# Kernel tuning notes

Hardware: AMD Instinct MI355X
Metric: run time of the kernel (lower is better)

Reference implementation:

```python
import jax, jax.numpy as jnp
import numpy as np

N_NODES = 100000
N_EDGES = 3200000
IN_DIM, HD_DIM, OUT_DIM = 128, 64, 32


def setup_inputs() -> dict:
    key = jax.random.key(0)
    ks = jax.random.split(key, 8)
    x = jax.random.normal(ks[0], (N_NODES, IN_DIM), dtype=jnp.float32)
    drop_u = jax.random.uniform(ks[1], (N_NODES, IN_DIM), dtype=jnp.float32)
    adj_val = jax.random.uniform(ks[2], (N_EDGES,), dtype=jnp.float32)
    adj_row = jax.random.randint(ks[3], (N_EDGES,), 0, N_NODES, dtype=jnp.int32)
    adj_col = jax.random.randint(ks[4], (N_EDGES,), 0, N_NODES, dtype=jnp.int32)
    W0 = jax.random.normal(ks[5], (IN_DIM, HD_DIM), dtype=jnp.float32) * (1.0 / np.sqrt(IN_DIM))
    b0 = jnp.zeros((HD_DIM,), dtype=jnp.float32)
    W1 = jax.random.normal(ks[6], (HD_DIM, OUT_DIM), dtype=jnp.float32) * (1.0 / np.sqrt(HD_DIM))
    b1 = jnp.zeros((OUT_DIM,), dtype=jnp.float32)
    return {"x": x, "drop_u": drop_u, "adj_val": adj_val, "adj_row": adj_row,
            "adj_col": adj_col, "W0": W0, "b0": b0, "W1": W1, "b1": b1}


def _spmm(val, row, col, h):
    # sparse [N,N] @ dense [N,D]: out[i] = sum_{e: row[e]=i} val[e] * h[col[e]]
    gathered = val[:, None] * h[col]          # [E, D] irregular gather
    return jax.ops.segment_sum(gathered, row, num_segments=N_NODES)


def reference(x, drop_u, adj_val, adj_row, adj_col, W0, b0, W1, b1):
    # dropout p=0.5 (training): keep where u >= 0.5, scale by 1/(1-p)=2
    mask = (drop_u >= 0.5).astype(x.dtype) * 2.0
    h = x * mask
    h = h @ W0 + b0                     # li0: [N, hd]
    h = _spmm(adj_val, adj_row, adj_col, h)
    h = jax.nn.relu(h)
    h = h @ W1 + b1                     # li1: [N, out]
    out = _spmm(adj_val, adj_row, adj_col, h)
    return out
```

## Files before the change

kernel.cpp:

```cpp
#include <hip/hip_runtime.h>

#define NN 100000
#define NE 3200000
#define EB 4096
#define NBP 782
#define BSH 9
#define BRW 512
#define NBK 196
#define CAP 17408

typedef short short8 __attribute__((ext_vector_type(8)));
typedef float f32x4 __attribute__((ext_vector_type(4)));

static __device__ __forceinline__ unsigned short f2bf(float f) {
  union { float f; unsigned int u; } c; c.f = f;
  unsigned int r = c.u + 0x7FFFu + ((c.u >> 16) & 1u);
  return (unsigned short)(r >> 16);
}
static __device__ __forceinline__ float lo16(unsigned int w) {
  union { unsigned int u; float f; } c; c.u = w << 16; return c.f;
}
static __device__ __forceinline__ float hi16(unsigned int w) {
  union { unsigned int u; float f; } c; c.u = w & 0xFFFF0000u; return c.f;
}


__global__ __launch_bounds__(256) void k_binit(int* __restrict__ bcur) {
  int t = threadIdx.x;
  if (t < NBK) bcur[t] = t * CAP;
}

__global__ __launch_bounds__(512) void k_part(const int* __restrict__ row,
                                              const int* __restrict__ col,
                                              const float* __restrict__ val,
                                              int* __restrict__ bcur,
                                              uint2* __restrict__ tmp) {
  __shared__ uint2 stage[EB];
  __shared__ int dst[EB];
  __shared__ int h[NBK];
  __shared__ int bex[NBK];
  __shared__ int win[NBK];
  __shared__ int c2[NBK];
  __shared__ int sc[512];
  int t = threadIdx.x;
  int e0 = blockIdx.x * EB;
  int n = min(EB, NE - e0);
  if (t < NBK) { h[t] = 0; c2[t] = 0; }
  __syncthreads();
  for (int i = t; i < n; i += 512) atomicAdd(&h[row[e0 + i] >> BSH], 1);
  __syncthreads();
  int v = (t < NBK) ? h[t] : 0;
  sc[t] = v;
  __syncthreads();
  for (int off = 1; off < 512; off <<= 1) {
    int a = (t >= off) ? sc[t - off] : 0;
    __syncthreads();
    sc[t] += a;
    __syncthreads();
  }
  int ex = sc[t] - v;
  if (t < NBK) {
    bex[t] = ex;
    win[t] = v ? atomicAdd(&bcur[t], v) : 0;
  }
  __syncthreads();
  for (int i = t; i < n; i += 512) {
    int e = e0 + i;
    int r = row[e];
    unsigned int c = (unsigned int)col[e];
    float vv = val[e];
    int b = r >> BSH;
    int rank = atomicAdd(&c2[b], 1);
    int s_ = bex[b] + rank;
    uint2 w;
    w.x = __float_as_uint(vv);
    w.y = ((unsigned int)(r & (BRW - 1)) << 17) | c;
    stage[s_] = w;
    dst[s_] = win[b] + rank;
  }
  __syncthreads();
  for (int i = t; i < n; i += 512) tmp[dst[i]] = stage[i];
}

__global__ __launch_bounds__(1024) void k_bsort(const int* __restrict__ bcur,
                                                const uint2* __restrict__ tmp,
                                                uint2* __restrict__ vc,
                                                int* __restrict__ rps,
                                                int* __restrict__ rpe) {
  __shared__ int cnt[BRW];
  __shared__ int pre[BRW];
  __shared__ int c2[BRW];
  int t = threadIdx.x;
  int b = blockIdx.x;
  int s0 = b * CAP;
  int n = bcur[b] - s0;
  if (t < BRW) { cnt[t] = 0; c2[t] = 0; }
  __syncthreads();
  const unsigned int* tmpy = (const unsigned int*)tmp;
  for (int i = t; i < n; i += 1024)
    atomicAdd(&cnt[tmpy[2 * (s0 + i) + 1] >> 17], 1);
  __syncthreads();
  int v = (t < BRW) ? cnt[t] : 0;
  if (t < BRW) pre[t] = v;
  __syncthreads();
  for (int off = 1; off < BRW; off <<= 1) {
    int a = (t >= off && t < BRW) ? pre[t - off] : 0;
    __syncthreads();
    if (t < BRW) pre[t] += a;
    __syncthreads();
  }
  if (t < BRW) {
    int ex = pre[t] - v;
    int r = (b << BSH) + t;
    if (r < NN) { rps[r] = s0 + ex; rpe[r] = s0 + ex + v; }
    pre[t] = ex;
  }
  __syncthreads();
  for (int i = t; i < n; i += 1024) {
    uint2 w = tmp[s0 + i];
    int rl = (int)(w.y >> 17);
    int rank = atomicAdd(&c2[rl], 1);
    int pos = s0 + pre[rl] + rank;
    uint2 o;
    o.x = w.x;
    o.y = w.y & 0x1FFFFu;
    vc[pos] = o;
  }
}

__global__ __launch_bounds__(256) void k_wcvt(const float* __restrict__ W0,
                                              unsigned short* __restrict__ W0bT,
                                              const float* __restrict__ W1,
                                              unsigned short* __restrict__ W1bT) {
  int idx = blockIdx.x * 256 + threadIdx.x;
  if (idx < 8192) {
    int n = idx >> 7, k = idx & 127;
    W0bT[idx] = f2bf(W0[(size_t)k * 64 + n]);
  } else if (idx < 8192 + 2048) {
    int i2 = idx - 8192;
    int n = i2 >> 6, k = i2 & 63;
    W1bT[i2] = f2bf(W1[(size_t)k * 32 + n]);
  }
}


__global__ __launch_bounds__(256) void k_gemm0(const float* __restrict__ x,
                                               const float* __restrict__ u,
                                               const unsigned short* __restrict__ W0bT,
                                               const float* __restrict__ b0,
                                               unsigned short* __restrict__ h0b) {
  __shared__ unsigned short xs[64][136];
  int t = threadIdx.x;
  int r0 = blockIdx.x * 64;
#pragma unroll
  for (int i = 0; i < 8; ++i) {
    int f4 = t + i * 256;
    int row = f4 >> 5;
    int off = f4 & 31;
    int r = r0 + row;
    float4 m = make_float4(0.f, 0.f, 0.f, 0.f);
    if (r < NN) {
      float4 xv = ((const float4*)(x + (size_t)r * 128))[off];
      float4 uv = ((const float4*)(u + (size_t)r * 128))[off];
      m.x = (uv.x >= 0.5f) ? xv.x : 0.f;
      m.y = (uv.y >= 0.5f) ? xv.y : 0.f;
      m.z = (uv.z >= 0.5f) ? xv.z : 0.f;
      m.w = (uv.w >= 0.5f) ? xv.w : 0.f;
    }
    uint2 pk;
    pk.x = (unsigned int)f2bf(m.x) | ((unsigned int)f2bf(m.y) << 16);
    pk.y = (unsigned int)f2bf(m.z) | ((unsigned int)f2bf(m.w) << 16);
    *(uint2*)&xs[row][off * 4] = pk;
  }
  __syncthreads();

  int lane = t & 63;
  int wv = __builtin_amdgcn_readfirstlane(t >> 6);
  int arow = wv * 16 + (lane & 15);
  int kgrp = lane >> 4;
  int ncol = lane & 15;

  short8 afrag[4];
#pragma unroll
  for (int kb = 0; kb < 4; ++kb)
    afrag[kb] = *(const short8*)&xs[arow][kgrp * 8 + kb * 32];

  short8 bfrag[4][4];
#pragma unroll
  for (int kb = 0; kb < 4; ++kb)
#pragma unroll
    for (int nb = 0; nb < 4; ++nb)
      bfrag[kb][nb] = *(const short8*)&W0bT[(size_t)(nb * 16 + ncol) * 128 +
                                            kgrp * 8 + kb * 32];

  f32x4 acc[4];
#pragma unroll
  for (int nb = 0; nb < 4; ++nb) acc[nb] = (f32x4)(0.f);
#pragma unroll
  for (int kb = 0; kb < 4; ++kb)
#pragma unroll
    for (int nb = 0; nb < 4; ++nb)
      acc[nb] = __builtin_amdgcn_mfma_f32_16x16x32_bf16(afrag[kb], bfrag[kb][nb],
                                                        acc[nb], 0, 0, 0);

#pragma unroll
  for (int nb = 0; nb < 4; ++nb) {
    int c = nb * 16 + ncol;
    float bias = b0[c];
#pragma unroll
    for (int reg = 0; reg < 4; ++reg) {
      int rr = r0 + wv * 16 + kgrp * 4 + reg;
      if (rr < NN) h0b[(size_t)rr * 64 + c] = f2bf(2.f * acc[nb][reg] + bias);
    }
  }
}


__global__ __launch_bounds__(256) void k_gemm1(const unsigned short* __restrict__ s1b,
                                               const unsigned short* __restrict__ W1bT,
                                               const float* __restrict__ b1,
                                               unsigned short* __restrict__ h1b) {
  __shared__ unsigned short ss[64][72];
  int t = threadIdx.x;
  int r0 = blockIdx.x * 64;
#pragma unroll
  for (int i = 0; i < 2; ++i) {
    int q = t + i * 256;
    int row = q >> 3;
    int off = q & 7;
    int r = r0 + row;
    uint4 w = make_uint4(0u, 0u, 0u, 0u);
    if (r < NN) w = ((const uint4*)(s1b + (size_t)r * 64))[off];
    *(uint4*)&ss[row][off * 8] = w;
  }
  __syncthreads();

  int lane = t & 63;
  int wv = __builtin_amdgcn_readfirstlane(t >> 6);
  int arow = wv * 16 + (lane & 15);
  int kgrp = lane >> 4;
  int ncol = lane & 15;

  short8 afrag[2];
#pragma unroll
  for (int kb = 0; kb < 2; ++kb)
    afrag[kb] = *(const short8*)&ss[arow][kgrp * 8 + kb * 32];

  short8 bfrag[2][2];
#pragma unroll
  for (int kb = 0; kb < 2; ++kb)
#pragma unroll
    for (int nb = 0; nb < 2; ++nb)
      bfrag[kb][nb] = *(const short8*)&W1bT[(size_t)(nb * 16 + ncol) * 64 +
                                            kgrp * 8 + kb * 32];

  f32x4 acc[2];
#pragma unroll
  for (int nb = 0; nb < 2; ++nb) acc[nb] = (f32x4)(0.f);
#pragma unroll
  for (int kb = 0; kb < 2; ++kb)
#pragma unroll
    for (int nb = 0; nb < 2; ++nb)
      acc[nb] = __builtin_amdgcn_mfma_f32_16x16x32_bf16(afrag[kb], bfrag[kb][nb],
                                                        acc[nb], 0, 0, 0);

#pragma unroll
  for (int nb = 0; nb < 2; ++nb) {
    int c = nb * 16 + ncol;
    float bias = b1[c];
#pragma unroll
    for (int reg = 0; reg < 4; ++reg) {
      int rr = r0 + wv * 16 + kgrp * 4 + reg;
      if (rr < NN) h1b[(size_t)rr * 32 + c] = f2bf(acc[nb][reg] + bias);
    }
  }
}


__global__ __launch_bounds__(256) void k_spmm1(const int* __restrict__ rps,
                                               const int* __restrict__ rpe,
                                               const uint2* __restrict__ vc,
                                               const uint2* __restrict__ h0v,
                                               uint2* __restrict__ s1v) {
  int wid = (blockIdx.x * 256 + threadIdx.x) >> 6;
  int lane = threadIdx.x & 63;
  if (wid >= NN) return;
  int qw = lane >> 4;
  int d = lane & 15;
  int j0 = rps[wid], j1 = rpe[wid];
  float a0 = 0.f, a1 = 0.f, a2 = 0.f, a3 = 0.f;
  int j = j0 + qw;
  uint2 e0, e1, e2, e3;
  bool have = (j + 12 < j1);
  if (have) { e0 = vc[j]; e1 = vc[j + 4]; e2 = vc[j + 8]; e3 = vc[j + 12]; }
  while (have) {
    uint2 g0 = h0v[(size_t)e0.y * 16 + d];
    uint2 g1 = h0v[(size_t)e1.y * 16 + d];
    uint2 g2 = h0v[(size_t)e2.y * 16 + d];
    uint2 g3 = h0v[(size_t)e3.y * 16 + d];
    float v0 = __uint_as_float(e0.x), v1 = __uint_as_float(e1.x);
    float v2 = __uint_as_float(e2.x), v3 = __uint_as_float(e3.x);
    int jn = j + 16;
    bool hn = (jn + 12 < j1);
    if (hn) { e0 = vc[jn]; e1 = vc[jn + 4]; e2 = vc[jn + 8]; e3 = vc[jn + 12]; }
    a0 = fmaf(v0, lo16(g0.x), a0); a1 = fmaf(v0, hi16(g0.x), a1);
    a2 = fmaf(v0, lo16(g0.y), a2); a3 = fmaf(v0, hi16(g0.y), a3);
    a0 = fmaf(v1, lo16(g1.x), a0); a1 = fmaf(v1, hi16(g1.x), a1);
    a2 = fmaf(v1, lo16(g1.y), a2); a3 = fmaf(v1, hi16(g1.y), a3);
    a0 = fmaf(v2, lo16(g2.x), a0); a1 = fmaf(v2, hi16(g2.x), a1);
    a2 = fmaf(v2, lo16(g2.y), a2); a3 = fmaf(v2, hi16(g2.y), a3);
    a0 = fmaf(v3, lo16(g3.x), a0); a1 = fmaf(v3, hi16(g3.x), a1);
    a2 = fmaf(v3, lo16(g3.y), a2); a3 = fmaf(v3, hi16(g3.y), a3);
    j = jn; have = hn;
  }
  for (; j < j1; j += 4) {
    uint2 e = vc[j];
    uint2 g = h0v[(size_t)e.y * 16 + d];
    float v = __uint_as_float(e.x);
    a0 = fmaf(v, lo16(g.x), a0); a1 = fmaf(v, hi16(g.x), a1);
    a2 = fmaf(v, lo16(g.y), a2); a3 = fmaf(v, hi16(g.y), a3);
  }
  a0 += __shfl_xor(a0, 16); a0 += __shfl_xor(a0, 32);
  a1 += __shfl_xor(a1, 16); a1 += __shfl_xor(a1, 32);
  a2 += __shfl_xor(a2, 16); a2 += __shfl_xor(a2, 32);
  a3 += __shfl_xor(a3, 16); a3 += __shfl_xor(a3, 32);
  if (qw == 0) {
    uint2 pk;
    pk.x = (unsigned int)f2bf(fmaxf(a0, 0.f)) | ((unsigned int)f2bf(fmaxf(a1, 0.f)) << 16);
    pk.y = (unsigned int)f2bf(fmaxf(a2, 0.f)) | ((unsigned int)f2bf(fmaxf(a3, 0.f)) << 16);
    s1v[(size_t)wid * 16 + d] = pk;
  }
}

__global__ __launch_bounds__(256) void k_spmm2(const int* __restrict__ rps,
                                               const int* __restrict__ rpe,
                                               const uint2* __restrict__ vc,
                                               const uint2* __restrict__ h1v,
                                               float* __restrict__ out) {
  int wid = (blockIdx.x * 256 + threadIdx.x) >> 6;
  int lane = threadIdx.x & 63;
  if (wid >= NN) return;
  int slot = lane >> 3;
  int d = lane & 7;
  int j0 = rps[wid], j1 = rpe[wid];
  float a0 = 0.f, a1 = 0.f, a2 = 0.f, a3 = 0.f;
  int j = j0 + slot;
  uint2 e0, e1;
  bool have = (j + 8 < j1);
  if (have) { e0 = vc[j]; e1 = vc[j + 8]; }
  while (have) {
    uint2 g0 = h1v[(size_t)e0.y * 8 + d];
    uint2 g1 = h1v[(size_t)e1.y * 8 + d];
    float v0 = __uint_as_float(e0.x), v1 = __uint_as_float(e1.x);
    int jn = j + 16;
    bool hn = (jn + 8 < j1);
    if (hn) { e0 = vc[jn]; e1 = vc[jn + 8]; }
    a0 = fmaf(v0, lo16(g0.x), a0); a1 = fmaf(v0, hi16(g0.x), a1);
    a2 = fmaf(v0, lo16(g0.y), a2); a3 = fmaf(v0, hi16(g0.y), a3);
    a0 = fmaf(v1, lo16(g1.x), a0); a1 = fmaf(v1, hi16(g1.x), a1);
    a2 = fmaf(v1, lo16(g1.y), a2); a3 = fmaf(v1, hi16(g1.y), a3);
    j = jn; have = hn;
  }
  for (; j < j1; j += 8) {
    uint2 e = vc[j];
    uint2 g = h1v[(size_t)e.y * 8 + d];
    float v = __uint_as_float(e.x);
    a0 = fmaf(v, lo16(g.x), a0); a1 = fmaf(v, hi16(g.x), a1);
    a2 = fmaf(v, lo16(g.y), a2); a3 = fmaf(v, hi16(g.y), a3);
  }
  a0 += __shfl_xor(a0, 8); a0 += __shfl_xor(a0, 16); a0 += __shfl_xor(a0, 32);
  a1 += __shfl_xor(a1, 8); a1 += __shfl_xor(a1, 16); a1 += __shfl_xor(a1, 32);
  a2 += __shfl_xor(a2, 8); a2 += __shfl_xor(a2, 16); a2 += __shfl_xor(a2, 32);
  a3 += __shfl_xor(a3, 8); a3 += __shfl_xor(a3, 16); a3 += __shfl_xor(a3, 32);
  if (slot == 0) {
    ((float4*)(out + (size_t)wid * 32))[d] = make_float4(a0, a1, a2, a3);
  }
}


extern "C" void kernel_launch(void* const* d_in, const int* in_sizes, int n_in,
                              void* d_out, int out_size, void* d_ws, size_t ws_size,
                              hipStream_t stream) {
  const float* x   = (const float*)d_in[0];
  const float* u   = (const float*)d_in[1];
  const float* val = (const float*)d_in[2];
  const int* row   = (const int*)d_in[3];
  const int* col   = (const int*)d_in[4];
  const float* W0  = (const float*)d_in[5];
  const float* b0  = (const float*)d_in[6];
  const float* W1  = (const float*)d_in[7];
  const float* b1  = (const float*)d_in[8];
  float* out = (float*)d_out;

  char* p = (char*)d_ws;
  auto take = [&](size_t bytes) {
    char* q = p;
    p += (bytes + 255) & ~(size_t)255;
    return q;
  };
  uint2* tmp = (uint2*)take((size_t)NBK * CAP * 8);
  uint2* vc  = (uint2*)take((size_t)NBK * CAP * 8);
  unsigned short* s1b = (unsigned short*)take((size_t)NN * 64 * 2);
  int* rps   = (int*)take((size_t)NN * 4);
  int* rpe   = (int*)take((size_t)NN * 4);
  int* bcur  = (int*)take((size_t)NBK * 4);
  unsigned short* w0bt = (unsigned short*)take((size_t)64 * 128 * 2);
  unsigned short* w1bt = (unsigned short*)take((size_t)32 * 64 * 2);
  unsigned short* h0b = (unsigned short*)tmp;
  unsigned short* h1b = (unsigned short*)((char*)tmp + (size_t)NN * 64 * 2);

  k_binit<<<1, 256, 0, stream>>>(bcur);
  k_part<<<NBP, 512, 0, stream>>>(row, col, val, bcur, tmp);
  k_bsort<<<NBK, 1024, 0, stream>>>(bcur, tmp, vc, rps, rpe);

  k_wcvt<<<40, 256, 0, stream>>>(W0, w0bt, W1, w1bt);
  k_gemm0<<<(NN + 63) / 64, 256, 0, stream>>>(x, u, w0bt, b0, h0b);
  k_spmm1<<<(NN + 3) / 4, 256, 0, stream>>>(rps, rpe, vc, (const uint2*)h0b,
                                            (uint2*)s1b);
  k_gemm1<<<(NN + 63) / 64, 256, 0, stream>>>(s1b, w1bt, b1, h1b);
  k_spmm2<<<(NN + 3) / 4, 256, 0, stream>>>(rps, rpe, vc, (const uint2*)h1b, out);
}
```

Baseline: 218.2 us.

## Process two rows per wavefront in SpMMs and use finer partition buckets

Each SpMM wavefront now handles two rows at once, interleaving their gathers so twice as many independent loads are in flight per wave, which targets gather latency. Separately, the row partition goes from 196 buckets of 512 rows to 782 buckets of 128 rows, with a paired-element scan in k_part and 512-thread k_bsort blocks, giving the bucket sort more blocks and less work per block. Costs include more registers per thread, imbalance when the two rows differ in degree, and the per-bucket capacity (4608) leaving less headroom over the expected ~4096 edges per bucket, which could overflow on skewed inputs.

```diff
diff --git a/kernel.cpp b/kernel.cpp
--- a/kernel.cpp
+++ b/kernel.cpp
@@ -4,10 +4,11 @@
 #define NE 3200000
 #define EB 4096
 #define NBP 782
-#define BSH 9
-#define BRW 512
-#define NBK 196
-#define CAP 17408
+#define BSH 7
+#define BRW 128
+#define NBK 782
+#define NBK2 784
+#define CAP 4608
 
 typedef short short8 __attribute__((ext_vector_type(8)));
 typedef float f32x4 __attribute__((ext_vector_type(4)));
@@ -26,7 +27,7 @@
 
 
 __global__ __launch_bounds__(256) void k_binit(int* __restrict__ bcur) {
-  int t = threadIdx.x;
+  int t = blockIdx.x * 256 + threadIdx.x;
   if (t < NBK) bcur[t] = t * CAP;
 }
 
@@ -37,20 +38,23 @@
                                               uint2* __restrict__ tmp) {
   __shared__ uint2 stage[EB];
   __shared__ int dst[EB];
-  __shared__ int h[NBK];
-  __shared__ int bex[NBK];
-  __shared__ int win[NBK];
-  __shared__ int c2[NBK];
+  __shared__ int h[NBK2];
+  __shared__ int bex[NBK2];
+  __shared__ int win[NBK2];
+  __shared__ int c2[NBK2];
   __shared__ int sc[512];
   int t = threadIdx.x;
   int e0 = blockIdx.x * EB;
   int n = min(EB, NE - e0);
-  if (t < NBK) { h[t] = 0; c2[t] = 0; }
+  for (int k = t; k < NBK2; k += 512) { h[k] = 0; c2[k] = 0; }
   __syncthreads();
   for (int i = t; i < n; i += 512) atomicAdd(&h[row[e0 + i] >> BSH], 1);
   __syncthreads();
-  int v = (t < NBK) ? h[t] : 0;
-  sc[t] = v;
+  int k0 = 2 * t, k1 = 2 * t + 1;
+  int v0 = (t < 392) ? h[k0] : 0;
+  int v1 = (t < 392) ? h[k1] : 0;
+  int s = v0 + v1;
+  sc[t] = s;
   __syncthreads();
   for (int off = 1; off < 512; off <<= 1) {
     int a = (t >= off) ? sc[t - off] : 0;
@@ -58,10 +62,12 @@
     sc[t] += a;
     __syncthreads();
   }
-  int ex = sc[t] - v;
-  if (t < NBK) {
-    bex[t] = ex;
-    win[t] = v ? atomicAdd(&bcur[t], v) : 0;
+  int ex = sc[t] - s;
+  if (t < 392) {
+    bex[k0] = ex;
+    bex[k1] = ex + v0;
+    win[k0] = v0 ? atomicAdd(&bcur[k0], v0) : 0;
+    win[k1] = v1 ? atomicAdd(&bcur[k1], v1) : 0;
   }
   __syncthreads();
   for (int i = t; i < n; i += 512) {
@@ -82,11 +88,11 @@
   for (int i = t; i < n; i += 512) tmp[dst[i]] = stage[i];
 }
 
-__global__ __launch_bounds__(1024) void k_bsort(const int* __restrict__ bcur,
-                                                const uint2* __restrict__ tmp,
-                                                uint2* __restrict__ vc,
-                                                int* __restrict__ rps,
-                                                int* __restrict__ rpe) {
+__global__ __launch_bounds__(512) void k_bsort(const int* __restrict__ bcur,
+                                               const uint2* __restrict__ tmp,
+                                               uint2* __restrict__ vc,
+                                               int* __restrict__ rps,
+                                               int* __restrict__ rpe) {
   __shared__ int cnt[BRW];
   __shared__ int pre[BRW];
   __shared__ int c2[BRW];
@@ -97,8 +103,7 @@
   if (t < BRW) { cnt[t] = 0; c2[t] = 0; }
   __syncthreads();
   const unsigned int* tmpy = (const unsigned int*)tmp;
-  for (int i = t; i < n; i += 1024)
-    atomicAdd(&cnt[tmpy[2 * (s0 + i) + 1] >> 17], 1);
+  for (int i = t; i < n; i += 512) atomicAdd(&cnt[tmpy[2 * (s0 + i) + 1] >> 17], 1);
   __syncthreads();
   int v = (t < BRW) ? cnt[t] : 0;
   if (t < BRW) pre[t] = v;
@@ -116,7 +121,7 @@
     pre[t] = ex;
   }
   __syncthreads();
-  for (int i = t; i < n; i += 1024) {
+  for (int i = t; i < n; i += 512) {
     uint2 w = tmp[s0 + i];
     int rl = (int)(w.y >> 17);
     int rank = atomicAdd(&c2[rl], 1);
@@ -282,27 +287,61 @@
                                                const uint2* __restrict__ vc,
                                                const uint2* __restrict__ h0v,
                                                uint2* __restrict__ s1v) {
-  int wid = (blockIdx.x * 256 + threadIdx.x) >> 6;
+  int wv = (blockIdx.x * 256 + threadIdx.x) >> 6;
   int lane = threadIdx.x & 63;
-  if (wid >= NN) return;
+  int rA = wv * 2;
+  if (rA >= NN) return;
+  int rB = rA + 1;
+  bool hasB = (rB < NN);
   int qw = lane >> 4;
   int d = lane & 15;
-  int j0 = rps[wid], j1 = rpe[wid];
+  int jA = rps[rA] + qw, jA1 = rpe[rA];
+  int jB = hasB ? (rps[rB] + qw) : 0, jB1 = hasB ? rpe[rB] : 0;
   float a0 = 0.f, a1 = 0.f, a2 = 0.f, a3 = 0.f;
-  int j = j0 + qw;
-  uint2 e0, e1, e2, e3;
-  bool have = (j + 12 < j1);
-  if (have) { e0 = vc[j]; e1 = vc[j + 4]; e2 = vc[j + 8]; e3 = vc[j + 12]; }
-  while (have) {
-    uint2 g0 = h0v[(size_t)e0.y * 16 + d];
-    uint2 g1 = h0v[(size_t)e1.y * 16 + d];
-    uint2 g2 = h0v[(size_t)e2.y * 16 + d];
-    uint2 g3 = h0v[(size_t)e3.y * 16 + d];
-    float v0 = __uint_as_float(e0.x), v1 = __uint_as_float(e1.x);
-    float v2 = __uint_as_float(e2.x), v3 = __uint_as_float(e3.x);
-    int jn = j + 16;
-    bool hn = (jn + 12 < j1);
-    if (hn) { e0 = vc[jn]; e1 = vc[jn + 4]; e2 = vc[jn + 8]; e3 = vc[jn + 12]; }
+  float c0 = 0.f, c1 = 0.f, c2 = 0.f, c3 = 0.f;
+  uint2 eA0, eA1, eA2, eA3, eB0, eB1, eB2, eB3;
+  bool hvA = (jA + 12 < jA1);
+  bool hvB = (jB + 12 < jB1);
+  if (hvA) { eA0 = vc[jA]; eA1 = vc[jA + 4]; eA2 = vc[jA + 8]; eA3 = vc[jA + 12]; }
+  if (hvB) { eB0 = vc[jB]; eB1 = vc[jB + 4]; eB2 = vc[jB + 8]; eB3 = vc[jB + 12]; }
+  while (hvA && hvB) {
+    uint2 gA0 = h0v[(size_t)eA0.y * 16 + d], gA1 = h0v[(size_t)eA1.y * 16 + d];
+    uint2 gA2 = h0v[(size_t)eA2.y * 16 + d], gA3 = h0v[(size_t)eA3.y * 16 + d];
+    uint2 gB0 = h0v[(size_t)eB0.y * 16 + d], gB1 = h0v[(size_t)eB1.y * 16 + d];
+    uint2 gB2 = h0v[(size_t)eB2.y * 16 + d], gB3 = h0v[(size_t)eB3.y * 16 + d];
+    float vA0 = __uint_as_float(eA0.x), vA1 = __uint_as_float(eA1.x);
+    float vA2 = __uint_as_float(eA2.x), vA3 = __uint_as_float(eA3.x);
+    float vB0 = __uint_as_float(eB0.x), vB1 = __uint_as_float(eB1.x);
+    float vB2 = __uint_as_float(eB2.x), vB3 = __uint_as_float(eB3.x);
+    jA += 16; jB += 16;
+    hvA = (jA + 12 < jA1); hvB = (jB + 12 < jB1);
+    if (hvA) { eA0 = vc[jA]; eA1 = vc[jA + 4]; eA2 = vc[jA + 8]; eA3 = vc[jA + 12]; }
+    if (hvB) { eB0 = vc[jB]; eB1 = vc[jB + 4]; eB2 = vc[jB + 8]; eB3 = vc[jB + 12]; }
+    a0 = fmaf(vA0, lo16(gA0.x), a0); a1 = fmaf(vA0, hi16(gA0.x), a1);
+    a2 = fmaf(vA0, lo16(gA0.y), a2); a3 = fmaf(vA0, hi16(gA0.y), a3);
+    a0 = fmaf(vA1, lo16(gA1.x), a0); a1 = fmaf(vA1, hi16(gA1.x), a1);
+    a2 = fmaf(vA1, lo16(gA1.y), a2); a3 = fmaf(vA1, hi16(gA1.y), a3);
+    a0 = fmaf(vA2, lo16(gA2.x), a0); a1 = fmaf(vA2, hi16(gA2.x), a1);
+    a2 = fmaf(vA2, lo16(gA2.y), a2); a3 = fmaf(vA2, hi16(gA2.y), a3);
+    a0 = fmaf(vA3, lo16(gA3.x), a0); a1 = fmaf(vA3, hi16(gA3.x), a1);
+    a2 = fmaf(vA3, lo16(gA3.y), a2); a3 = fmaf(vA3, hi16(gA3.y), a3);
+    c0 = fmaf(vB0, lo16(gB0.x), c0); c1 = fmaf(vB0, hi16(gB0.x), c1);
+    c2 = fmaf(vB0, lo16(gB0.y), c2); c3 = fmaf(vB0, hi16(gB0.y), c3);
+    c0 = fmaf(vB1, lo16(gB1.x), c0); c1 = fmaf(vB1, hi16(gB1.x), c1);
+    c2 = fmaf(vB1, lo16(gB1.y), c2); c3 = fmaf(vB1, hi16(gB1.y), c3);
+    c0 = fmaf(vB2, lo16(gB2.x), c0); c1 = fmaf(vB2, hi16(gB2.x), c1);
+    c2 = fmaf(vB2, lo16(gB2.y), c2); c3 = fmaf(vB2, hi16(gB2.y), c3);
+    c0 = fmaf(vB3, lo16(gB3.x), c0); c1 = fmaf(vB3, hi16(gB3.x), c1);
+    c2 = fmaf(vB3, lo16(gB3.y), c2); c3 = fmaf(vB3, hi16(gB3.y), c3);
+  }
+  while (hvA) {
+    uint2 g0 = h0v[(size_t)eA0.y * 16 + d], g1 = h0v[(size_t)eA1.y * 16 + d];
+    uint2 g2 = h0v[(size_t)eA2.y * 16 + d], g3 = h0v[(size_t)eA3.y * 16 + d];
+    float v0 = __uint_as_float(eA0.x), v1 = __uint_as_float(eA1.x);
+    float v2 = __uint_as_float(eA2.x), v3 = __uint_as_float(eA3.x);
+    jA += 16;
+    hvA = (jA + 12 < jA1);
+    if (hvA) { eA0 = vc[jA]; eA1 = vc[jA + 4]; eA2 = vc[jA + 8]; eA3 = vc[jA + 12]; }
     a0 = fmaf(v0, lo16(g0.x), a0); a1 = fmaf(v0, hi16(g0.x), a1);
     a2 = fmaf(v0, lo16(g0.y), a2); a3 = fmaf(v0, hi16(g0.y), a3);
     a0 = fmaf(v1, lo16(g1.x), a0); a1 = fmaf(v1, hi16(g1.x), a1);
@@ -311,24 +350,56 @@
     a2 = fmaf(v2, lo16(g2.y), a2); a3 = fmaf(v2, hi16(g2.y), a3);
     a0 = fmaf(v3, lo16(g3.x), a0); a1 = fmaf(v3, hi16(g3.x), a1);
     a2 = fmaf(v3, lo16(g3.y), a2); a3 = fmaf(v3, hi16(g3.y), a3);
-    j = jn; have = hn;
-  }
-  for (; j < j1; j += 4) {
-    uint2 e = vc[j];
+  }
+  while (hvB) {
+    uint2 g0 = h0v[(size_t)eB0.y * 16 + d], g1 = h0v[(size_t)eB1.y * 16 + d];
+    uint2 g2 = h0v[(size_t)eB2.y * 16 + d], g3 = h0v[(size_t)eB3.y * 16 + d];
+    float v0 = __uint_as_float(eB0.x), v1 = __uint_as_float(eB1.x);
+    float v2 = __uint_as_float(eB2.x), v3 = __uint_as_float(eB3.x);
+    jB += 16;
+    hvB = (jB + 12 < jB1);
+    if (hvB) { eB0 = vc[jB]; eB1 = vc[jB + 4]; eB2 = vc[jB + 8]; eB3 = vc[jB + 12]; }
+    c0 = fmaf(v0, lo16(g0.x), c0); c1 = fmaf(v0, hi16(g0.x), c1);
+    c2 = fmaf(v0, lo16(g0.y), c2); c3 = fmaf(v0, hi16(g0.y), c3);
+    c0 = fmaf(v1, lo16(g1.x), c0); c1 = fmaf(v1, hi16(g1.x), c1);
+    c2 = fmaf(v1, lo16(g1.y), c2); c3 = fmaf(v1, hi16(g1.y), c3);
+    c0 = fmaf(v2, lo16(g2.x), c0); c1 = fmaf(v2, hi16(g2.x), c1);
+    c2 = fmaf(v2, lo16(g2.y), c2); c3 = fmaf(v2, hi16(g2.y), c3);
+    c0 = fmaf(v3, lo16(g3.x), c0); c1 = fmaf(v3, hi16(g3.x), c1);
+    c2 = fmaf(v3, lo16(g3.y), c2); c3 = fmaf(v3, hi16(g3.y), c3);
+  }
+  for (; jA < jA1; jA += 4) {
+    uint2 e = vc[jA];
     uint2 g = h0v[(size_t)e.y * 16 + d];
     float v = __uint_as_float(e.x);
     a0 = fmaf(v, lo16(g.x), a0); a1 = fmaf(v, hi16(g.x), a1);
     a2 = fmaf(v, lo16(g.y), a2); a3 = fmaf(v, hi16(g.y), a3);
   }
+  for (; jB < jB1; jB += 4) {
+    uint2 e = vc[jB];
+    uint2 g = h0v[(size_t)e.y * 16 + d];
+    float v = __uint_as_float(e.x);
+    c0 = fmaf(v, lo16(g.x), c0); c1 = fmaf(v, hi16(g.x), c1);
+    c2 = fmaf(v, lo16(g.y), c2); c3 = fmaf(v, hi16(g.y), c3);
+  }
   a0 += __shfl_xor(a0, 16); a0 += __shfl_xor(a0, 32);
   a1 += __shfl_xor(a1, 16); a1 += __shfl_xor(a1, 32);
   a2 += __shfl_xor(a2, 16); a2 += __shfl_xor(a2, 32);
   a3 += __shfl_xor(a3, 16); a3 += __shfl_xor(a3, 32);
+  c0 += __shfl_xor(c0, 16); c0 += __shfl_xor(c0, 32);
+  c1 += __shfl_xor(c1, 16); c1 += __shfl_xor(c1, 32);
+  c2 += __shfl_xor(c2, 16); c2 += __shfl_xor(c2, 32);
+  c3 += __shfl_xor(c3, 16); c3 += __shfl_xor(c3, 32);
   if (qw == 0) {
     uint2 pk;
     pk.x = (unsigned int)f2bf(fmaxf(a0, 0.f)) | ((unsigned int)f2bf(fmaxf(a1, 0.f)) << 16);
     pk.y = (unsigned int)f2bf(fmaxf(a2, 0.f)) | ((unsigned int)f2bf(fmaxf(a3, 0.f)) << 16);
-    s1v[(size_t)wid * 16 + d] = pk;
+    s1v[(size_t)rA * 16 + d] = pk;
+  } else if (qw == 1 && hasB) {
+    uint2 pk;
+    pk.x = (unsigned int)f2bf(fmaxf(c0, 0.f)) | ((unsigned int)f2bf(fmaxf(c1, 0.f)) << 16);
+    pk.y = (unsigned int)f2bf(fmaxf(c2, 0.f)) | ((unsigned int)f2bf(fmaxf(c3, 0.f)) << 16);
+    s1v[(size_t)rB * 16 + d] = pk;
   }
 }
 
@@ -337,43 +408,89 @@
                                                const uint2* __restrict__ vc,
                                                const uint2* __restrict__ h1v,
                                                float* __restrict__ out) {
-  int wid = (blockIdx.x * 256 + threadIdx.x) >> 6;
+  int wv = (blockIdx.x * 256 + threadIdx.x) >> 6;
   int lane = threadIdx.x & 63;
-  if (wid >= NN) return;
+  int rA = wv * 2;
+  if (rA >= NN) return;
+  int rB = rA + 1;
+  bool hasB = (rB < NN);
   int slot = lane >> 3;
   int d = lane & 7;
-  int j0 = rps[wid], j1 = rpe[wid];
+  int jA = rps[rA] + slot, jA1 = rpe[rA];
+  int jB = hasB ? (rps[rB] + slot) : 0, jB1 = hasB ? rpe[rB] : 0;
   float a0 = 0.f, a1 = 0.f, a2 = 0.f, a3 = 0.f;
-  int j = j0 + slot;
-  uint2 e0, e1;
-  bool have = (j + 8 < j1);
-  if (have) { e0 = vc[j]; e1 = vc[j + 8]; }
-  while (have) {
-    uint2 g0 = h1v[(size_t)e0.y * 8 + d];
-    uint2 g1 = h1v[(size_t)e1.y * 8 + d];
-    float v0 = __uint_as_float(e0.x), v1 = __uint_as_float(e1.x);
-    int jn = j + 16;
-    bool hn = (jn + 8 < j1);
-    if (hn) { e0 = vc[jn]; e1 = vc[jn + 8]; }
+  float c0 = 0.f, c1 = 0.f, c2 = 0.f, c3 = 0.f;
+  uint2 eA0, eA1, eB0, eB1;
+  bool hvA = (jA + 8 < jA1);
+  bool hvB = (jB + 8 < jB1);
+  if (hvA) { eA0 = vc[jA]; eA1 = vc[jA + 8]; }
+  if (hvB) { eB0 = vc[jB]; eB1 = vc[jB + 8]; }
+  while (hvA && hvB) {
+    uint2 gA0 = h1v[(size_t)eA0.y * 8 + d], gA1 = h1v[(size_t)eA1.y * 8 + d];
+    uint2 gB0 = h1v[(size_t)eB0.y * 8 + d], gB1 = h1v[(size_t)eB1.y * 8 + d];
+    float vA0 = __uint_as_float(eA0.x), vA1 = __uint_as_float(eA1.x);
+    float vB0 = __uint_as_float(eB0.x), vB1 = __uint_as_float(eB1.x);
+    jA += 16; jB += 16;
+    hvA = (jA + 8 < jA1); hvB = (jB + 8 < jB1);
+    if (hvA) { eA0 = vc[jA]; eA1 = vc[jA + 8]; }
+    if (hvB) { eB0 = vc[jB]; eB1 = vc[jB + 8]; }
+    a0 = fmaf(vA0, lo16(gA0.x), a0); a1 = fmaf(vA0, hi16(gA0.x), a1);
+    a2 = fmaf(vA0, lo16(gA0.y), a2); a3 = fmaf(vA0, hi16(gA0.y), a3);
+    a0 = fmaf(vA1, lo16(gA1.x), a0); a1 = fmaf(vA1, hi16(gA1.x), a1);
+    a2 = fmaf(vA1, lo16(gA1.y), a2); a3 = fmaf(vA1, hi16(gA1.y), a3);
+    c0 = fmaf(vB0, lo16(gB0.x), c0); c1 = fmaf(vB0, hi16(gB0.x), c1);
+    c2 = fmaf(vB0, lo16(gB0.y), c2); c3 = fmaf(vB0, hi16(gB0.y), c3);
+    c0 = fmaf(vB1, lo16(gB1.x), c0); c1 = fmaf(vB1, hi16(gB1.x), c1);
+    c2 = fmaf(vB1, lo16(gB1.y), c2); c3 = fmaf(vB1, hi16(gB1.y), c3);
+  }
+  while (hvA) {
+    uint2 g0 = h1v[(size_t)eA0.y * 8 + d], g1 = h1v[(size_t)eA1.y * 8 + d];
+    float v0 = __uint_as_float(eA0.x), v1 = __uint_as_float(eA1.x);
+    jA += 16;
+    hvA = (jA + 8 < jA1);
+    if (hvA) { eA0 = vc[jA]; eA1 = vc[jA + 8]; }
     a0 = fmaf(v0, lo16(g0.x), a0); a1 = fmaf(v0, hi16(g0.x), a1);
     a2 = fmaf(v0, lo16(g0.y), a2); a3 = fmaf(v0, hi16(g0.y), a3);
     a0 = fmaf(v1, lo16(g1.x), a0); a1 = fmaf(v1, hi16(g1.x), a1);
     a2 = fmaf(v1, lo16(g1.y), a2); a3 = fmaf(v1, hi16(g1.y), a3);
-    j = jn; have = hn;
-  }
-  for (; j < j1; j += 8) {
-    uint2 e = vc[j];
+  }
+  while (hvB) {
+    uint2 g0 = h1v[(size_t)eB0.y * 8 + d], g1 = h1v[(size_t)eB1.y * 8 + d];
+    float v0 = __uint_as_float(eB0.x), v1 = __uint_as_float(eB1.x);
+    jB += 16;
+    hvB = (jB + 8 < jB1);
+    if (hvB) { eB0 = vc[jB]; eB1 = vc[jB + 8]; }
+    c0 = fmaf(v0, lo16(g0.x), c0); c1 = fmaf(v0, hi16(g0.x), c1);
+    c2 = fmaf(v0, lo16(g0.y), c2); c3 = fmaf(v0, hi16(g0.y), c3);
+    c0 = fmaf(v1, lo16(g1.x), c0); c1 = fmaf(v1, hi16(g1.x), c1);
+    c2 = fmaf(v1, lo16(g1.y), c2); c3 = fmaf(v1, hi16(g1.y), c3);
+  }
+  for (; jA < jA1; jA += 8) {
+    uint2 e = vc[jA];
     uint2 g = h1v[(size_t)e.y * 8 + d];
     float v = __uint_as_float(e.x);
     a0 = fmaf(v, lo16(g.x), a0); a1 = fmaf(v, hi16(g.x), a1);
     a2 = fmaf(v, lo16(g.y), a2); a3 = fmaf(v, hi16(g.y), a3);
   }
+  for (; jB < jB1; jB += 8) {
+    uint2 e = vc[jB];
+    uint2 g = h1v[(size_t)e.y * 8 + d];
+    float v = __uint_as_float(e.x);
+    c0 = fmaf(v, lo16(g.x), c0); c1 = fmaf(v, hi16(g.x), c1);
+    c2 = fmaf(v, lo16(g.y), c2); c3 = fmaf(v, hi16(g.y), c3);
+  }
   a0 += __shfl_xor(a0, 8); a0 += __shfl_xor(a0, 16); a0 += __shfl_xor(a0, 32);
   a1 += __shfl_xor(a1, 8); a1 += __shfl_xor(a1, 16); a1 += __shfl_xor(a1, 32);
   a2 += __shfl_xor(a2, 8); a2 += __shfl_xor(a2, 16); a2 += __shfl_xor(a2, 32);
   a3 += __shfl_xor(a3, 8); a3 += __shfl_xor(a3, 16); a3 += __shfl_xor(a3, 32);
+  c0 += __shfl_xor(c0, 8); c0 += __shfl_xor(c0, 16); c0 += __shfl_xor(c0, 32);
+  c1 += __shfl_xor(c1, 8); c1 += __shfl_xor(c1, 16); c1 += __shfl_xor(c1, 32);
+  c2 += __shfl_xor(c2, 8); c2 += __shfl_xor(c2, 16); c2 += __shfl_xor(c2, 32);
+  c3 += __shfl_xor(c3, 8); c3 += __shfl_xor(c3, 16); c3 += __shfl_xor(c3, 32);
   if (slot == 0) {
-    ((float4*)(out + (size_t)wid * 32))[d] = make_float4(a0, a1, a2, a3);
+    ((float4*)(out + (size_t)rA * 32))[d] = make_float4(a0, a1, a2, a3);
+  } else if (slot == 1 && hasB) {
+    ((float4*)(out + (size_t)rB * 32))[d] = make_float4(c0, c1, c2, c3);
   }
 }
 
@@ -409,14 +526,14 @@
   unsigned short* h0b = (unsigned short*)tmp;
   unsigned short* h1b = (unsigned short*)((char*)tmp + (size_t)NN * 64 * 2);
 
-  k_binit<<<1, 256, 0, stream>>>(bcur);
+  k_binit<<<(NBK + 255) / 256, 256, 0, stream>>>(bcur);
   k_part<<<NBP, 512, 0, stream>>>(row, col, val, bcur, tmp);
-  k_bsort<<<NBK, 1024, 0, stream>>>(bcur, tmp, vc, rps, rpe);
+  k_bsort<<<NBK, 512, 0, stream>>>(bcur, tmp, vc, rps, rpe);
 
   k_wcvt<<<40, 256, 0, stream>>>(W0, w0bt, W1, w1bt);
   k_gemm0<<<(NN + 63) / 64, 256, 0, stream>>>(x, u, w0bt, b0, h0b);
-  k_spmm1<<<(NN + 3) / 4, 256, 0, stream>>>(rps, rpe, vc, (const uint2*)h0b,
+  k_spmm1<<<(NN + 7) / 8, 256, 0, stream>>>(rps, rpe, vc, (const uint2*)h0b,
                                             (uint2*)s1b);
   k_gemm1<<<(NN + 63) / 64, 256, 0, stream>>>(s1b, w1bt, b1, h1b);
-  k_spmm2<<<(NN + 3) / 4, 256, 0, stream>>>(rps, rpe, vc, (const uint2*)h1b, out);
-}
+  k_spmm2<<<(NN + 7) / 8, 256, 0, stream>>>(rps, rpe, vc, (const uint2*)h1b, out);
+}
```

After: 249.3 us. 1.14x slower.

## Split feature dimension into 16-column panels for cache-resident SpMM gathers

Applied to the files above, without the earlier changes.

The GEMM kernels now write h0/h1 in column-panel layout (16 bf16 columns per panel, panel-major), and each SpMM runs as multiple launches, one per panel. Each panel is 3.2 MB, which fits in L2, so the random gathers by column index should hit cache instead of HBM. The cost is re-reading the edge list (vc) once per panel: four times for the first SpMM and twice for the second. It also adds extra launches, and each gather now moves only 32 bytes per edge.

```diff
diff --git a/kernel.cpp b/kernel.cpp
--- a/kernel.cpp
+++ b/kernel.cpp
@@ -210,7 +210,8 @@
 #pragma unroll
     for (int reg = 0; reg < 4; ++reg) {
       int rr = r0 + wv * 16 + kgrp * 4 + reg;
-      if (rr < NN) h0b[(size_t)rr * 64 + c] = f2bf(2.f * acc[nb][reg] + bias);
+      if (rr < NN)
+        h0b[((size_t)nb * NN + rr) * 16 + ncol] = f2bf(2.f * acc[nb][reg] + bias);
     }
   }
 }
@@ -271,109 +272,99 @@
 #pragma unroll
     for (int reg = 0; reg < 4; ++reg) {
       int rr = r0 + wv * 16 + kgrp * 4 + reg;
-      if (rr < NN) h1b[(size_t)rr * 32 + c] = f2bf(acc[nb][reg] + bias);
+      if (rr < NN)
+        h1b[((size_t)nb * NN + rr) * 16 + ncol] = f2bf(acc[nb][reg] + bias);
     }
   }
 }
 
 
-__global__ __launch_bounds__(256) void k_spmm1(const int* __restrict__ rps,
-                                               const int* __restrict__ rpe,
-                                               const uint2* __restrict__ vc,
-                                               const uint2* __restrict__ h0v,
-                                               uint2* __restrict__ s1v) {
+__global__ __launch_bounds__(256) void k_spmm1p(const int* __restrict__ rps,
+                                                const int* __restrict__ rpe,
+                                                const uint2* __restrict__ vc,
+                                                const uint2* __restrict__ h0s,
+                                                uint2* __restrict__ s1v,
+                                                int p) {
   int wid = (blockIdx.x * 256 + threadIdx.x) >> 6;
   int lane = threadIdx.x & 63;
   if (wid >= NN) return;
-  int qw = lane >> 4;
-  int d = lane & 15;
+  int slot = lane >> 2;
+  int d = lane & 3;
   int j0 = rps[wid], j1 = rpe[wid];
   float a0 = 0.f, a1 = 0.f, a2 = 0.f, a3 = 0.f;
-  int j = j0 + qw;
-  uint2 e0, e1, e2, e3;
-  bool have = (j + 12 < j1);
-  if (have) { e0 = vc[j]; e1 = vc[j + 4]; e2 = vc[j + 8]; e3 = vc[j + 12]; }
+  int j = j0;
+  uint2 e;
+  bool have = (j + 15 < j1);
+  if (have) e = vc[j + slot];
   while (have) {
-    uint2 g0 = h0v[(size_t)e0.y * 16 + d];
-    uint2 g1 = h0v[(size_t)e1.y * 16 + d];
-    uint2 g2 = h0v[(size_t)e2.y * 16 + d];
-    uint2 g3 = h0v[(size_t)e3.y * 16 + d];
-    float v0 = __uint_as_float(e0.x), v1 = __uint_as_float(e1.x);
-    float v2 = __uint_as_float(e2.x), v3 = __uint_as_float(e3.x);
+    uint2 g = h0s[(size_t)e.y * 4 + d];
+    float v = __uint_as_float(e.x);
     int jn = j + 16;
-    bool hn = (jn + 12 < j1);
-    if (hn) { e0 = vc[jn]; e1 = vc[jn + 4]; e2 = vc[jn + 8]; e3 = vc[jn + 12]; }
-    a0 = fmaf(v0, lo16(g0.x), a0); a1 = fmaf(v0, hi16(g0.x), a1);
-    a2 = fmaf(v0, lo16(g0.y), a2); a3 = fmaf(v0, hi16(g0.y), a3);
-    a0 = fmaf(v1, lo16(g1.x), a0); a1 = fmaf(v1, hi16(g1.x), a1);
-    a2 = fmaf(v1, lo16(g1.y), a2); a3 = fmaf(v1, hi16(g1.y), a3);
-    a0 = fmaf(v2, lo16(g2.x), a0); a1 = fmaf(v2, hi16(g2.x), a1);
-    a2 = fmaf(v2, lo16(g2.y), a2); a3 = fmaf(v2, hi16(g2.y), a3);
-    a0 = fmaf(v3, lo16(g3.x), a0); a1 = fmaf(v3, hi16(g3.x), a1);
-    a2 = fmaf(v3, lo16(g3.y), a2); a3 = fmaf(v3, hi16(g3.y), a3);
-    j = jn; have = hn;
-  }
-  for (; j < j1; j += 4) {
-    uint2 e = vc[j];
-    uint2 g = h0v[(size_t)e.y * 16 + d];
-    float v = __uint_as_float(e.x);
+    bool hn = (jn + 15 < j1);
+    if (hn) e = vc[jn + slot];
     a0 = fmaf(v, lo16(g.x), a0); a1 = fmaf(v, hi16(g.x), a1);
     a2 = fmaf(v, lo16(g.y), a2); a3 = fmaf(v, hi16(g.y), a3);
-  }
-  a0 += __shfl_xor(a0, 16); a0 += __shfl_xor(a0, 32);
-  a1 += __shfl_xor(a1, 16); a1 += __shfl_xor(a1, 32);
-  a2 += __shfl_xor(a2, 16); a2 += __shfl_xor(a2, 32);
-  a3 += __shfl_xor(a3, 16); a3 += __shfl_xor(a3, 32);
-  if (qw == 0) {
+    j = jn; have = hn;
+  }
+  if (j + slot < j1) {
+    uint2 et = vc[j + slot];
+    uint2 g = h0s[(size_t)et.y * 4 + d];
+    float v = __uint_as_float(et.x);
+    a0 = fmaf(v, lo16(g.x), a0); a1 = fmaf(v, hi16(g.x), a1);
+    a2 = fmaf(v, lo16(g.y), a2); a3 = fmaf(v, hi16(g.y), a3);
+  }
+  a0 += __shfl_xor(a0, 4); a0 += __shfl_xor(a0, 8); a0 += __shfl_xor(a0, 16); a0 += __shfl_xor(a0, 32);
+  a1 += __shfl_xor(a1, 4); a1 += __shfl_xor(a1, 8); a1 += __shfl_xor(a1, 16); a1 += __shfl_xor(a1, 32);
+  a2 += __shfl_xor(a2, 4); a2 += __shfl_xor(a2, 8); a2 += __shfl_xor(a2, 16); a2 += __shfl_xor(a2, 32);
+  a3 += __shfl_xor(a3, 4); a3 += __shfl_xor(a3, 8); a3 += __shfl_xor(a3, 16); a3 += __shfl_xor(a3, 32);
+  if (lane < 4) {
     uint2 pk;
     pk.x = (unsigned int)f2bf(fmaxf(a0, 0.f)) | ((unsigned int)f2bf(fmaxf(a1, 0.f)) << 16);
     pk.y = (unsigned int)f2bf(fmaxf(a2, 0.f)) | ((unsigned int)f2bf(fmaxf(a3, 0.f)) << 16);
-    s1v[(size_t)wid * 16 + d] = pk;
-  }
-}
-
-__global__ __launch_bounds__(256) void k_spmm2(const int* __restrict__ rps,
-                                               const int* __restrict__ rpe,
-                                               const uint2* __restrict__ vc,
-                                               const uint2* __restrict__ h1v,
-                                               float* __restrict__ out) {
+    s1v[(size_t)wid * 16 + p * 4 + d] = pk;
+  }
+}
+
+__global__ __launch_bounds__(256) void k_spmm2p(const int* __restrict__ rps,
+                                                const int* __restrict__ rpe,
+                                                const uint2* __restrict__ vc,
+                                                const uint2* __restrict__ h1s,
+                                                float* __restrict__ out,
+                                                int p) {
   int wid = (blockIdx.x * 256 + threadIdx.x) >> 6;
   int lane = threadIdx.x & 63;
   if (wid >= NN) return;
-  int slot = lane >> 3;
-  int d = lane & 7;
+  int slot = lane >> 2;
+  int d = lane & 3;
   int j0 = rps[wid], j1 = rpe[wid];
   float a0 = 0.f, a1 = 0.f, a2 = 0.f, a3 = 0.f;
-  int j = j0 + slot;
-  uint2 e0, e1;
-  bool have = (j + 8 < j1);
-  if (have) { e0 = vc[j]; e1 = vc[j + 8]; }
+  int j = j0;
+  uint2 e;
+  bool have = (j + 15 < j1);
+  if (have) e = vc[j + slot];
   while (have) {
-    uint2 g0 = h1v[(size_t)e0.y * 8 + d];
-    uint2 g1 = h1v[(size_t)e1.y * 8 + d];
-    float v0 = __uint_as_float(e0.x), v1 = __uint_as_float(e1.x);
+    uint2 g = h1s[(size_t)e.y * 4 + d];
+    float v = __uint_as_float(e.x);
     int jn = j + 16;
-    bool hn = (jn + 8 < j1);
-    if (hn) { e0 = vc[jn]; e1 = vc[jn + 8]; }
-    a0 = fmaf(v0, lo16(g0.x), a0); a1 = fmaf(v0, hi16(g0.x), a1);
-    a2 = fmaf(v0, lo16(g0.y), a2); a3 = fmaf(v0, hi16(g0.y), a3);
-    a0 = fmaf(v1, lo16(g1.x), a0); a1 = fmaf(v1, hi16(g1.x), a1);
-    a2 = fmaf(v1, lo16(g1.y), a2); a3 = fmaf(v1, hi16(g1.y), a3);
-    j = jn; have = hn;
-  }
-  for (; j < j1; j += 8) {
-    uint2 e = vc[j];
-    uint2 g = h1v[(size_t)e.y * 8 + d];
-    float v = __uint_as_float(e.x);
+    bool hn = (jn + 15 < j1);
+    if (hn) e = vc[jn + slot];
     a0 = fmaf(v, lo16(g.x), a0); a1 = fmaf(v, hi16(g.x), a1);
     a2 = fmaf(v, lo16(g.y), a2); a3 = fmaf(v, hi16(g.y), a3);
-  }
-  a0 += __shfl_xor(a0, 8); a0 += __shfl_xor(a0, 16); a0 += __shfl_xor(a0, 32);
-  a1 += __shfl_xor(a1, 8); a1 += __shfl_xor(a1, 16); a1 += __shfl_xor(a1, 32);
-  a2 += __shfl_xor(a2, 8); a2 += __shfl_xor(a2, 16); a2 += __shfl_xor(a2, 32);
-  a3 += __shfl_xor(a3, 8); a3 += __shfl_xor(a3, 16); a3 += __shfl_xor(a3, 32);
-  if (slot == 0) {
-    ((float4*)(out + (size_t)wid * 32))[d] = make_float4(a0, a1, a2, a3);
+    j = jn; have = hn;
+  }
+  if (j + slot < j1) {
+    uint2 et = vc[j + slot];
+    uint2 g = h1s[(size_t)et.y * 4 + d];
+    float v = __uint_as_float(et.x);
+    a0 = fmaf(v, lo16(g.x), a0); a1 = fmaf(v, hi16(g.x), a1);
+    a2 = fmaf(v, lo16(g.y), a2); a3 = fmaf(v, hi16(g.y), a3);
+  }
+  a0 += __shfl_xor(a0, 4); a0 += __shfl_xor(a0, 8); a0 += __shfl_xor(a0, 16); a0 += __shfl_xor(a0, 32);
+  a1 += __shfl_xor(a1, 4); a1 += __shfl_xor(a1, 8); a1 += __shfl_xor(a1, 16); a1 += __shfl_xor(a1, 32);
+  a2 += __shfl_xor(a2, 4); a2 += __shfl_xor(a2, 8); a2 += __shfl_xor(a2, 16); a2 += __shfl_xor(a2, 32);
+  a3 += __shfl_xor(a3, 4); a3 += __shfl_xor(a3, 8); a3 += __shfl_xor(a3, 16); a3 += __shfl_xor(a3, 32);
+  if (lane < 4) {
+    ((float4*)out)[(size_t)wid * 8 + p * 4 + d] = make_float4(a0, a1, a2, a3);
   }
 }
 
@@ -415,8 +406,13 @@
 
   k_wcvt<<<40, 256, 0, stream>>>(W0, w0bt, W1, w1bt);
   k_gemm0<<<(NN + 63) / 64, 256, 0, stream>>>(x, u, w0bt, b0, h0b);
-  k_spmm1<<<(NN + 3) / 4, 256, 0, stream>>>(rps, rpe, vc, (const uint2*)h0b,
-                                            (uint2*)s1b);
+  for (int ps = 0; ps < 4; ++ps) {
+    const uint2* h0s = (const uint2*)(h0b + (size_t)ps * NN * 16);
+    k_spmm1p<<<(NN + 3) / 4, 256, 0, stream>>>(rps, rpe, vc, h0s, (uint2*)s1b, ps);
+  }
   k_gemm1<<<(NN + 63) / 64, 256, 0, stream>>>(s1b, w1bt, b1, h1b);
-  k_spmm2<<<(NN + 3) / 4, 256, 0, stream>>>(rps, rpe, vc, (const uint2*)h1b, out);
-}
+  for (int ps = 0; ps < 2; ++ps) {
+    const uint2* h1s = (const uint2*)(h1b + (size_t)ps * NN * 16);
+    k_spmm2p<<<(NN + 3) / 4, 256, 0, stream>>>(rps, rpe, vc, h1s, out, ps);
+  }
+}
```

New measurement: 325.4 us. 49.1% more time.
